# Kernel tuning notes

Measured on AMD Instinct MI355X. Metric: run time of the kernel, lower is better.

The kernel has to match this reference:

```python
import jax, jax.numpy as jnp
import numpy as np

N_EMBED = 1024
N_HEAD = 16
HEAD_DIM = N_EMBED // N_HEAD


def setup_inputs() -> dict:
    key = jax.random.key(0)
    k1, k2, k3, k4, k5 = jax.random.split(key, 5)
    x = jax.random.normal(k1, (4, 2048, N_EMBED), dtype=jnp.float32)
    s = 1.0 / np.sqrt(N_EMBED)
    W_attn = jax.random.normal(k2, (N_EMBED, 3 * N_EMBED), dtype=jnp.float32) * s
    b_attn = jnp.zeros((3 * N_EMBED,), dtype=jnp.float32)
    W_proj = jax.random.normal(k3, (N_EMBED, N_EMBED), dtype=jnp.float32) * s
    b_proj = jnp.zeros((N_EMBED,), dtype=jnp.float32)
    return {"x": x, "W_attn": W_attn, "b_attn": b_attn, "W_proj": W_proj, "b_proj": b_proj}


def reference(x, W_attn, b_attn, W_proj, b_proj):
    B, T, C = x.shape
    qkv = x @ W_attn + b_attn  # [B, T, 3C]
    q, k, v = jnp.split(qkv, 3, axis=2)
    # [B, H, T, D]
    q = q.reshape(B, T, N_HEAD, HEAD_DIM).transpose(0, 2, 1, 3)
    k = k.reshape(B, T, N_HEAD, HEAD_DIM).transpose(0, 2, 1, 3)
    v = v.reshape(B, T, N_HEAD, HEAD_DIM).transpose(0, 2, 1, 3)
    scale = 1.0 / np.sqrt(HEAD_DIM)
    scores = jnp.einsum('bhqd,bhkd->bhqk', q, k) * scale
    causal = jnp.tril(jnp.ones((T, T), dtype=bool))
    scores = jnp.where(causal[None, None], scores, -jnp.inf)
    attn = jax.nn.softmax(scores, axis=-1)
    y = jnp.einsum('bhqk,bhkd->bhqd', attn, v)
    y = y.transpose(0, 2, 1, 3).reshape(B, T, C)
    return y @ W_proj + b_proj
```

## Files before the change

### kernel.cpp

```cpp
#include <hip/hip_runtime.h>

typedef unsigned short u16;
typedef unsigned int u32;
typedef unsigned long long u64;
typedef __attribute__((ext_vector_type(8))) __bf16 b8;
typedef __attribute__((ext_vector_type(4))) float f32x4;

#define T_SEQ 2048
#define NB 4
#define NH 16
#define HD 64
#define CEMB 1024
#define M_ROWS (NB * T_SEQ)
#define Q_PRESCALE 0.18033688011112042f

__device__ __forceinline__ u16 f2bf(float f) {
  union { float f; unsigned int u; } v; v.f = f;
  unsigned int r = v.u + 0x7FFFu + ((v.u >> 16) & 1u);
  return (u16)(r >> 16);
}

__device__ __forceinline__ u32 pk2bf(float a, float b) {
  __bf16 x = (__bf16)a, y = (__bf16)b;
  return (u32)*(u16*)&x | ((u32)*(u16*)&y << 16);
}

__device__ __forceinline__ void gl_lds16(const u16* g, u16* l) {
  __builtin_amdgcn_global_load_lds(
      (const __attribute__((address_space(1))) unsigned int*)g,
      (__attribute__((address_space(3))) unsigned int*)l, 16, 0, 0);
}

#define BARRIER() __builtin_amdgcn_s_barrier()
#define LGKM0() do { asm volatile("s_waitcnt lgkmcnt(0)" ::: "memory"); \
                     __builtin_amdgcn_sched_barrier(0); } while (0)
#define VMCNT4() asm volatile("s_waitcnt vmcnt(4)" ::: "memory")
#define VMCNT2() asm volatile("s_waitcnt vmcnt(2)" ::: "memory")
#define VMCNT0() asm volatile("s_waitcnt vmcnt(0)" ::: "memory")

__global__ void k_convert(const float* __restrict__ in, u16* __restrict__ out, int n4) {
  int i = blockIdx.x * blockDim.x + threadIdx.x;
  int stride = gridDim.x * blockDim.x;
  for (; i < n4; i += stride) {
    float4 v = ((const float4*)in)[i];
    ushort4 o;
    o.x = f2bf(v.x); o.y = f2bf(v.y); o.z = f2bf(v.z); o.w = f2bf(v.w);
    ((ushort4*)out)[i] = o;
  }
}

__global__ __launch_bounds__(256) void k_transpose(const float* __restrict__ W,
                                                   u16* __restrict__ Wt, int K, int N) {
  __shared__ u16 t[64][65];
  int k0 = blockIdx.y * 64, n0 = blockIdx.x * 64;
  int tx = threadIdx.x & 63, ty = threadIdx.x >> 6;
  for (int i = ty; i < 64; i += 4)
    t[i][tx] = f2bf(W[(size_t)(k0 + i) * N + n0 + tx]);
  __syncthreads();
  for (int i = ty; i < 64; i += 4)
    Wt[(size_t)(n0 + i) * K + k0 + tx] = t[tx][i];
}

template <int MODE, int BNU>
__global__ __launch_bounds__(512, 2) void k_gemm8(const u16* __restrict__ A,
                                                  const u16* __restrict__ Bt,
                                                  const float* __restrict__ bias,
                                                  u16* __restrict__ out_bf,
                                                  float* __restrict__ out_f,
                                                  u16* __restrict__ vt,
                                                  int M, int N, int K, int mstripe) {
  __shared__ u16 sA[2][16384];
  __shared__ u16 sB[2][BNU * 4096];
  constexpr int NI = BNU / 2;
  const int tid = threadIdx.x;
  const int lane = tid & 63;
  const int wid = tid >> 6;
  const int wm = wid >> 2;
  const int wn = wid & 3;
  const int fr = lane & 15;
  const int g = lane >> 4;

  const int xcd = blockIdx.x & 7;
  const int idx = blockIdx.x >> 3;
  const int mt = xcd * mstripe + (idx % mstripe);
  const int nt = idx / mstripe;
  const int row0 = mt * 256, col0 = nt * (BNU * 64);
  const int NT = K >> 6;

  const int kswz = ((lane & 7) ^ ((lane >> 3) & 7)) * 8;
  const u16* gA = A + (size_t)(row0 + wid * 8 + (lane >> 3)) * K + kswz;
  const u16* gB = Bt + (size_t)(col0 + wid * 8 + (lane >> 3)) * K + kswz;

#define SGA(buf, T, u) gl_lds16(gA + (size_t)(u) * 64 * K + (size_t)(T) * 64, \
                                &sA[buf][(u) * 4096 + wid * 512])
#define SGB(buf, T, u) gl_lds16(gB + (size_t)(u) * 64 * K + (size_t)(T) * 64, \
                                &sB[buf][(u) * 4096 + wid * 512])
#define RDA(dst, rowe, ks)                                                     \
  { int row_ = (rowe);                                                         \
    dst = *(const b8*)&sA[bufc][row_ * 64 + ((((ks)*4 + g) ^ (row_ & 7)) << 3)]; }
#define RDB(dst, cole, ks)                                                     \
  { int col_ = (cole);                                                         \
    dst = *(const b8*)&sB[bufc][col_ * 64 + ((((ks)*4 + g) ^ (col_ & 7)) << 3)]; }

  f32x4 acc[8][BNU] = {};
  b8 aF[4][2], bF0[NI][2], bF1[NI][2];

#pragma unroll
  for (int u = 0; u < BNU; ++u) SGB(0, 0, u);
  SGA(0, 0, 0); SGA(0, 0, 2);
  SGA(0, 0, 1); SGA(0, 0, 3);
  SGA(1, 1, 0); SGA(1, 1, 2);
  VMCNT4();
  BARRIER();
  __builtin_amdgcn_sched_barrier(0);

#pragma unroll 2
  for (int T = 0; T < NT; ++T) {
    const int bufc = T & 1, bufn = bufc ^ 1;
    const bool st1 = (T + 1 < NT), st2 = (T + 2 < NT);

#pragma unroll
    for (int mi = 0; mi < 4; ++mi)
#pragma unroll
      for (int ks = 0; ks < 2; ++ks) RDA(aF[mi][ks], wm * 128 + mi * 16 + fr, ks);
#pragma unroll
    for (int ni = 0; ni < NI; ++ni)
#pragma unroll
      for (int ks = 0; ks < 2; ++ks) RDB(bF0[ni][ks], wn * (BNU * 16) + ni * 16 + fr, ks);
    if (st1) { SGB(bufn, T + 1, 0); SGB(bufn, T + 1, 1); }
    else VMCNT0();
    BARRIER(); LGKM0();
    __builtin_amdgcn_s_setprio(1);
#pragma unroll
    for (int mi = 0; mi < 4; ++mi)
#pragma unroll
      for (int ni = 0; ni < NI; ++ni)
#pragma unroll
        for (int ks = 0; ks < 2; ++ks)
          acc[mi][ni] = __builtin_amdgcn_mfma_f32_16x16x32_bf16(aF[mi][ks], bF0[ni][ks], acc[mi][ni], 0, 0, 0);
    __builtin_amdgcn_s_setprio(0);
    __builtin_amdgcn_sched_barrier(0);
    BARRIER();

#pragma unroll
    for (int ni = 0; ni < NI; ++ni)
#pragma unroll
      for (int ks = 0; ks < 2; ++ks) RDB(bF1[ni][ks], wn * (BNU * 16) + (NI + ni) * 16 + fr, ks);
    if (BNU == 4 && st1) { SGB(bufn, T + 1, 2); SGB(bufn, T + 1, 3); }
    if constexpr (BNU == 4) { VMCNT4(); } else { VMCNT2(); }
    BARRIER(); LGKM0();
    __builtin_amdgcn_s_setprio(1);
#pragma unroll
    for (int mi = 0; mi < 4; ++mi)
#pragma unroll
      for (int ni = 0; ni < NI; ++ni)
#pragma unroll
        for (int ks = 0; ks < 2; ++ks)
          acc[mi][NI + ni] = __builtin_amdgcn_mfma_f32_16x16x32_bf16(aF[mi][ks], bF1[ni][ks], acc[mi][NI + ni], 0, 0, 0);
    __builtin_amdgcn_s_setprio(0);
    __builtin_amdgcn_sched_barrier(0);
    BARRIER();

#pragma unroll
    for (int mi = 0; mi < 4; ++mi)
#pragma unroll
      for (int ks = 0; ks < 2; ++ks) RDA(aF[mi][ks], wm * 128 + 64 + mi * 16 + fr, ks);
    if (st2) { SGA(bufc, T + 2, 0); SGA(bufc, T + 2, 2); }
    BARRIER(); LGKM0();
    __builtin_amdgcn_s_setprio(1);
#pragma unroll
    for (int mi = 0; mi < 4; ++mi)
#pragma unroll
      for (int ni = 0; ni < NI; ++ni)
#pragma unroll
        for (int ks = 0; ks < 2; ++ks)
          acc[4 + mi][ni] = __builtin_amdgcn_mfma_f32_16x16x32_bf16(aF[mi][ks], bF0[ni][ks], acc[4 + mi][ni], 0, 0, 0);
    __builtin_amdgcn_s_setprio(0);
    __builtin_amdgcn_sched_barrier(0);
    BARRIER();

    if (st1) { SGA(bufn, T + 1, 1); SGA(bufn, T + 1, 3); }
    VMCNT4();
    BARRIER();
    __builtin_amdgcn_sched_barrier(0);
    __builtin_amdgcn_s_setprio(1);
#pragma unroll
    for (int mi = 0; mi < 4; ++mi)
#pragma unroll
      for (int ni = 0; ni < NI; ++ni)
#pragma unroll
        for (int ks = 0; ks < 2; ++ks)
          acc[4 + mi][NI + ni] = __builtin_amdgcn_mfma_f32_16x16x32_bf16(aF[mi][ks], bF1[ni][ks], acc[4 + mi][NI + ni], 0, 0, 0);
    __builtin_amdgcn_s_setprio(0);
    __builtin_amdgcn_sched_barrier(0);
    BARRIER();
  }
#undef SGA
#undef SGB
#undef RDA
#undef RDB

  const int fg = lane >> 4;
  if (MODE != 2) {
#pragma unroll
    for (int ni = 0; ni < BNU; ++ni) {
      int col = col0 + wn * (BNU * 16) + ni * 16 + fr;
      float bv = bias[col];
#pragma unroll
      for (int mi = 0; mi < 8; ++mi) {
#pragma unroll
        for (int r = 0; r < 4; ++r) {
          int row = row0 + wm * 128 + mi * 16 + fg * 4 + r;
          float v = acc[mi][ni][r] + bv;
          if (MODE == 0) {
            float sc = (col < CEMB) ? Q_PRESCALE : 1.0f;
            out_bf[(size_t)row * (2 * CEMB) + col] = f2bf(v * sc);
          } else {
            out_f[(size_t)row * N + col] = v;
          }
        }
      }
    }
  } else {
    u16* st = (u16*)sA;
    const int bq = row0 >> 11;
    const int t0g = row0 & (T_SEQ - 1);
#pragma unroll
    for (int pass = 0; pass < 2; ++pass) {
      __syncthreads();
      if ((wn >> 1) == pass) {
#pragma unroll
        for (int nn = 0; nn < BNU; ++nn) {
          const int hdl = (wn & 1) * 32 + nn * 16 + fr;
          const float bv = bias[col0 + pass * 64 + hdl];
#pragma unroll
          for (int mi = 0; mi < 8; ++mi) {
            const int tl = wm * 128 + mi * 16 + fg * 4;
#pragma unroll
            for (int rp = 0; rp < 2; ++rp) {
              u32 pk = pk2bf(acc[mi][nn][2 * rp] + bv, acc[mi][nn][2 * rp + 1] + bv);
              *(u32*)&st[hdl * 280 + tl + 2 * rp] = pk;
            }
          }
        }
      }
      __syncthreads();
      const int hd_r = tid >> 3;
      const int ck = tid & 7;
      u16* vrow = vt + ((size_t)(bq * (NH * HD) + col0 + pass * 64 + hd_r)) * T_SEQ + t0g;
#pragma unroll
      for (int j = 0; j < 4; ++j) {
        const int chunk = ck + 8 * j;
        f32x4 d = *(const f32x4*)&st[hd_r * 280 + chunk * 8];
        *(f32x4*)&vrow[chunk * 8] = d;
      }
    }
  }
}

__global__ __launch_bounds__(256) void k_attn(const u16* __restrict__ qk,
                                              const u16* __restrict__ vtg,
                                              u16* __restrict__ y) {
  __shared__ __align__(16) u16 kt_s[2][64 * 64];
  __shared__ __align__(16) u16 vt_s[2][64 * 64];
  __shared__ __align__(16) char pl_s[4][2048];

  const int lane = threadIdx.x & 63;
  const int wave = threadIdx.x >> 6;
  const int tid = threadIdx.x;
  const int g = lane >> 4, c = lane & 15;

  const int xcd = blockIdx.x & 7;
  const int idx = blockIdx.x >> 3;
  const int bh = xcd * 8 + (idx & 7);
  const int pr = idx >> 3;
  const int b = bh >> 4, h = bh & 15;

  char* plw = pl_s[wave];
  char* plA = plw + c * 128;
  const int b3 = c >> 3;
  const int e2 = (c & 7) << 1;
  const int sb = g + b3 * 8;

  b8 ones_frag;
#pragma unroll
  for (int e = 0; e < 8; ++e) ones_frag[e] = (c == 0) ? (__bf16)1.0f : (__bf16)0.0f;

  const int srow = tid >> 3;
  const int scc = (tid & 7) ^ (srow & 7);
  const u16* ksrc0 = qk + ((size_t)(b * T_SEQ) + srow) * (2 * CEMB) + CEMB + h * HD + scc * 8;
  const u16* vsrc0 = vtg + ((size_t)(bh * HD) + srow) * T_SEQ + scc * 8;

#define STAGE(t, bb)                                                    \
  {                                                                     \
    const u16* ks_ = ksrc0 + (size_t)(t) * 64 * (2 * CEMB);             \
    const u16* vs_ = vsrc0 + (t) * 64;                                  \
    gl_lds16(ks_, &kt_s[bb][wave * 512]);                               \
    gl_lds16(ks_ + 32 * (2 * CEMB), &kt_s[bb][wave * 512 + 2048]);      \
    gl_lds16(vs_, &vt_s[bb][wave * 512]);                               \
    gl_lds16(vs_ + 32 * T_SEQ, &vt_s[bb][wave * 512 + 2048]);           \
  }

#pragma unroll 1
  for (int seg = 0; seg < 2; ++seg) {
    const int tt = seg ? pr : (15 - pr);
    const int qA = tt * 128 + wave * 16;
    const int qB = qA + 64;

    const u16* qrowA = qk + (size_t)(b * T_SEQ + qA + c) * (2 * CEMB) + h * HD + g * 8;
    const b8 qfA0 = *(const b8*)qrowA;
    const b8 qfA1 = *(const b8*)(qrowA + 32);
    const u16* qrowB = qrowA + (size_t)64 * (2 * CEMB);
    const b8 qfB0 = *(const b8*)qrowB;
    const b8 qfB1 = *(const b8*)(qrowB + 32);

    float mA = -3e38f, mB = -3e38f;
    f32x4 oA[4] = {}, oB[4] = {};
    f32x4 o4A = {0.f, 0.f, 0.f, 0.f}, o4B = {0.f, 0.f, 0.f, 0.f};

    const int nt_tiles = 2 * tt + 2;
    int cur = 0;
    STAGE(0, 0);
    __syncthreads();

    for (int t = 0; t < nt_tiles; ++t) {
      if (t + 1 < nt_tiles) STAGE(t + 1, cur ^ 1);
      const int k0 = t * 64;
      const bool lastt = (t == nt_tiles - 1);
      const bool sndl = (t == nt_tiles - 2);
      const u16* kt = kt_s[cur];
      const u16* vtl = vt_s[cur];

      f32x4 sA[4] = {{0.f,0.f,0.f,0.f},{0.f,0.f,0.f,0.f},{0.f,0.f,0.f,0.f},{0.f,0.f,0.f,0.f}};
      f32x4 sB[4] = {{0.f,0.f,0.f,0.f},{0.f,0.f,0.f,0.f},{0.f,0.f,0.f,0.f},{0.f,0.f,0.f,0.f}};
      __builtin_amdgcn_s_setprio(1);
#pragma unroll
      for (int n = 0; n < 4; ++n) {
        const bool needA = (!lastt) && (!sndl || n <= wave);
        const bool needB = (!lastt) || (n <= wave);
        if (needA || needB) {
          const b8 kf0 = *(const b8*)&kt[(n * 16 + c) * 64 + ((g ^ (c & 7)) << 3)];
          const b8 kf1 = *(const b8*)&kt[(n * 16 + c) * 64 + (((4 + g) ^ (c & 7)) << 3)];
          if (needA) {
            sA[n] = __builtin_amdgcn_mfma_f32_16x16x32_bf16(kf0, qfA0, sA[n], 0, 0, 0);
            sA[n] = __builtin_amdgcn_mfma_f32_16x16x32_bf16(kf1, qfA1, sA[n], 0, 0, 0);
          }
          if (needB) {
            sB[n] = __builtin_amdgcn_mfma_f32_16x16x32_bf16(kf0, qfB0, sB[n], 0, 0, 0);
            sB[n] = __builtin_amdgcn_mfma_f32_16x16x32_bf16(kf1, qfB1, sB[n], 0, 0, 0);
          }
        }
      }
      __builtin_amdgcn_s_setprio(0);

      if (sndl) {
#pragma unroll
        for (int n = 0; n < 4; ++n)
#pragma unroll
          for (int r = 0; r < 4; ++r)
            if (k0 + n * 16 + g * 4 + r > qA + c) sA[n][r] = -3e38f;
      }
      if (lastt) {
#pragma unroll
        for (int n = 0; n < 4; ++n)
#pragma unroll
          for (int r = 0; r < 4; ++r)
            if (k0 + n * 16 + g * 4 + r > qB + c) sB[n][r] = -3e38f;
      }

      float rmA = -3e38f, rmB = -3e38f;
      if (!lastt) {
#pragma unroll
        for (int n = 0; n < 4; ++n)
#pragma unroll
          for (int r = 0; r < 4; ++r) rmA = fmaxf(rmA, sA[n][r]);
        rmA = fmaxf(rmA, __shfl_xor(rmA, 16));
        rmA = fmaxf(rmA, __shfl_xor(rmA, 32));
      }
#pragma unroll
      for (int n = 0; n < 4; ++n)
#pragma unroll
        for (int r = 0; r < 4; ++r) rmB = fmaxf(rmB, sB[n][r]);
      rmB = fmaxf(rmB, __shfl_xor(rmB, 16));
      rmB = fmaxf(rmB, __shfl_xor(rmB, 32));

      bool ok = (lastt || rmA <= mA + 8.0f) && (rmB <= mB + 8.0f);
      if (!__all(ok)) {
        float alA = 1.0f, alB;
        if (!lastt) {
          float mn = fmaxf(mA, rmA);
          alA = __builtin_amdgcn_exp2f(mA - mn);
          mA = mn;
        }
        {
          float mn = fmaxf(mB, rmB);
          alB = __builtin_amdgcn_exp2f(mB - mn);
          mB = mn;
        }
#pragma unroll
        for (int r = 0; r < 4; ++r) {
          int src = (lane & 48) + g * 4 + r;
          float aA = __shfl(alA, src);
          float aB = __shfl(alB, src);
#pragma unroll
          for (int nt = 0; nt < 4; ++nt) { oA[nt][r] *= aA; oB[nt][r] *= aB; }
          o4A[r] *= aA; o4B[r] *= aB;
        }
      }

      if (!lastt) {
#pragma unroll
        for (int n = 0; n < 4; ++n) {
          u32 lo = pk2bf(__builtin_amdgcn_exp2f(sA[n][0] - mA),
                         __builtin_amdgcn_exp2f(sA[n][1] - mA));
          u32 hi = pk2bf(__builtin_amdgcn_exp2f(sA[n][2] - mA),
                         __builtin_amdgcn_exp2f(sA[n][3] - mA));
          *(u64*)(plA + ((((4 * n + sb) & 15) ^ e2) << 3)) = ((u64)hi << 32) | lo;
        }
      }
      u64 pbB[4];
#pragma unroll
      for (int n = 0; n < 4; ++n) {
        u32 lo = pk2bf(__builtin_amdgcn_exp2f(sB[n][0] - mB),
                       __builtin_amdgcn_exp2f(sB[n][1] - mB));
        u32 hi = pk2bf(__builtin_amdgcn_exp2f(sB[n][2] - mB),
                       __builtin_amdgcn_exp2f(sB[n][3] - mB));
        pbB[n] = ((u64)hi << 32) | lo;
      }

      b8 vb[2][4];
#pragma unroll
      for (int ks = 0; ks < 2; ++ks)
#pragma unroll
        for (int nt = 0; nt < 4; ++nt)
          vb[ks][nt] = *(const b8*)&vtl[(nt * 16 + c) * 64 + (((ks * 4 + g) ^ (c & 7)) << 3)];

      asm volatile("s_waitcnt lgkmcnt(0)" ::: "memory");
      __builtin_amdgcn_sched_barrier(0);

      if (!lastt) {
        __builtin_amdgcn_s_setprio(1);
#pragma unroll
        for (int ks = 0; ks < 2; ++ks) {
          const b8 paA = *(const b8*)(plA + ((((ks * 8 + 2 * g + 8 * b3) & 15) ^ e2) << 3));
          o4A = __builtin_amdgcn_mfma_f32_16x16x32_bf16(paA, ones_frag, o4A, 0, 0, 0);
#pragma unroll
          for (int nt = 0; nt < 4; ++nt)
            oA[nt] = __builtin_amdgcn_mfma_f32_16x16x32_bf16(paA, vb[ks][nt], oA[nt], 0, 0, 0);
        }
        __builtin_amdgcn_s_setprio(0);
      }

#pragma unroll
      for (int n = 0; n < 4; ++n)
        *(u64*)(plA + ((((4 * n + sb) & 15) ^ e2) << 3)) = pbB[n];
      asm volatile("s_waitcnt lgkmcnt(0)" ::: "memory");
      __builtin_amdgcn_sched_barrier(0);

      __builtin_amdgcn_s_setprio(1);
#pragma unroll
      for (int ks = 0; ks < 2; ++ks) {
        const b8 paB = *(const b8*)(plA + ((((ks * 8 + 2 * g + 8 * b3) & 15) ^ e2) << 3));
        o4B = __builtin_amdgcn_mfma_f32_16x16x32_bf16(paB, ones_frag, o4B, 0, 0, 0);
#pragma unroll
        for (int nt = 0; nt < 4; ++nt)
          oB[nt] = __builtin_amdgcn_mfma_f32_16x16x32_bf16(paB, vb[ks][nt], oB[nt], 0, 0, 0);
      }
      __builtin_amdgcn_s_setprio(0);

      __syncthreads();
      cur ^= 1;
    }

#pragma unroll
    for (int r = 0; r < 4; ++r) {
      float lA = __shfl(o4A[r], lane & 48);
      float lB = __shfl(o4B[r], lane & 48);
      float invA = 1.0f / lA;
      float invB = 1.0f / lB;
#pragma unroll
      for (int nt = 0; nt < 4; ++nt) {
        __bf16 va = (__bf16)(oA[nt][r] * invA);
        __bf16 vbv = (__bf16)(oB[nt][r] * invB);
        y[(size_t)(b * T_SEQ + qA + g * 4 + r) * CEMB + h * HD + nt * 16 + c] = *(u16*)&va;
        y[(size_t)(b * T_SEQ + qB + g * 4 + r) * CEMB + h * HD + nt * 16 + c] = *(u16*)&vbv;
      }
    }
  }
#undef STAGE
}

extern "C" void kernel_launch(void* const* d_in, const int* in_sizes, int n_in,
                              void* d_out, int out_size, void* d_ws, size_t ws_size,
                              hipStream_t stream) {
  const float* x = (const float*)d_in[0];
  const float* W_attn = (const float*)d_in[1];
  const float* b_attn = (const float*)d_in[2];
  const float* W_proj = (const float*)d_in[3];
  const float* b_proj = (const float*)d_in[4];
  float* out = (float*)d_out;

  char* ws = (char*)d_ws;
  u16* x_bf    = (u16*)(ws);
  u16* wattn_t = (u16*)(ws + 16777216);
  u16* wproj_t = (u16*)(ws + 23068672);
  u16* qk_bf   = (u16*)(ws + 25165824);
  u16* vt      = (u16*)(ws + 58720256);
  u16* y_bf    = (u16*)(ws + 75497472);

  k_convert<<<2048, 256, 0, stream>>>(x, x_bf, (NB * T_SEQ * CEMB) / 4);
  k_transpose<<<dim3(3 * CEMB / 64, CEMB / 64), 256, 0, stream>>>(W_attn, wattn_t, CEMB, 3 * CEMB);
  k_transpose<<<dim3(CEMB / 64, CEMB / 64), 256, 0, stream>>>(W_proj, wproj_t, CEMB, CEMB);
  k_gemm8<0, 4><<<256, 512, 0, stream>>>(x_bf, wattn_t, b_attn, qk_bf, nullptr, nullptr,
                                         M_ROWS, 2 * CEMB, CEMB, 4);
  k_gemm8<2, 2><<<256, 512, 0, stream>>>(x_bf, wattn_t + 2048 * CEMB, b_attn + 2 * CEMB,
                                         nullptr, nullptr, vt, M_ROWS, CEMB, CEMB, 4);
  k_attn<<<512, 256, 0, stream>>>(qk_bf, vt, y_bf);
  k_gemm8<1, 2><<<256, 512, 0, stream>>>(y_bf, wproj_t, b_proj, nullptr, out, nullptr,
                                         M_ROWS, CEMB, CEMB, 4);
}
```

Before: 194.1 us.

## Split attention blocks to one 64-row query tile per wave group

```diff
diff --git a/kernel.cpp b/kernel.cpp
--- a/kernel.cpp
+++ b/kernel.cpp
@@ -258,9 +258,9 @@
   }
 }
 
-__global__ __launch_bounds__(256) void k_attn(const u16* __restrict__ qk,
-                                              const u16* __restrict__ vtg,
-                                              u16* __restrict__ y) {
+__global__ __launch_bounds__(256, 4) void k_attn(const u16* __restrict__ qk,
+                                                 const u16* __restrict__ vtg,
+                                                 u16* __restrict__ y) {
   __shared__ __align__(16) u16 kt_s[2][64 * 64];
   __shared__ __align__(16) u16 vt_s[2][64 * 64];
   __shared__ __align__(16) char pl_s[4][2048];
@@ -303,129 +303,79 @@
 
 #pragma unroll 1
   for (int seg = 0; seg < 2; ++seg) {
-    const int tt = seg ? pr : (15 - pr);
-    const int qA = tt * 128 + wave * 16;
-    const int qB = qA + 64;
-
-    const u16* qrowA = qk + (size_t)(b * T_SEQ + qA + c) * (2 * CEMB) + h * HD + g * 8;
-    const b8 qfA0 = *(const b8*)qrowA;
-    const b8 qfA1 = *(const b8*)(qrowA + 32);
-    const u16* qrowB = qrowA + (size_t)64 * (2 * CEMB);
-    const b8 qfB0 = *(const b8*)qrowB;
-    const b8 qfB1 = *(const b8*)(qrowB + 32);
-
-    float mA = -3e38f, mB = -3e38f;
-    f32x4 oA[4] = {}, oB[4] = {};
-    f32x4 o4A = {0.f, 0.f, 0.f, 0.f}, o4B = {0.f, 0.f, 0.f, 0.f};
-
-    const int nt_tiles = 2 * tt + 2;
+    const int tt = seg ? pr : (31 - pr);
+    const int qW = tt * 64 + wave * 16;
+
+    const u16* qrow = qk + (size_t)(b * T_SEQ + qW + c) * (2 * CEMB) + h * HD + g * 8;
+    const b8 qf0 = *(const b8*)qrow;
+    const b8 qf1 = *(const b8*)(qrow + 32);
+
+    float m = -3e38f;
+    f32x4 o[4] = {};
+    f32x4 o4 = {0.f, 0.f, 0.f, 0.f};
+
+    const int ntt = tt + 1;
     int cur = 0;
     STAGE(0, 0);
     __syncthreads();
 
-    for (int t = 0; t < nt_tiles; ++t) {
-      if (t + 1 < nt_tiles) STAGE(t + 1, cur ^ 1);
+    for (int t = 0; t < ntt; ++t) {
+      if (t + 1 < ntt) STAGE(t + 1, cur ^ 1);
       const int k0 = t * 64;
-      const bool lastt = (t == nt_tiles - 1);
-      const bool sndl = (t == nt_tiles - 2);
+      const bool diag = (t == ntt - 1);
       const u16* kt = kt_s[cur];
       const u16* vtl = vt_s[cur];
 
-      f32x4 sA[4] = {{0.f,0.f,0.f,0.f},{0.f,0.f,0.f,0.f},{0.f,0.f,0.f,0.f},{0.f,0.f,0.f,0.f}};
-      f32x4 sB[4] = {{0.f,0.f,0.f,0.f},{0.f,0.f,0.f,0.f},{0.f,0.f,0.f,0.f},{0.f,0.f,0.f,0.f}};
+      f32x4 s[4] = {{0.f,0.f,0.f,0.f},{0.f,0.f,0.f,0.f},{0.f,0.f,0.f,0.f},{0.f,0.f,0.f,0.f}};
       __builtin_amdgcn_s_setprio(1);
 #pragma unroll
       for (int n = 0; n < 4; ++n) {
-        const bool needA = (!lastt) && (!sndl || n <= wave);
-        const bool needB = (!lastt) || (n <= wave);
-        if (needA || needB) {
+        if (!diag || n <= wave) {
           const b8 kf0 = *(const b8*)&kt[(n * 16 + c) * 64 + ((g ^ (c & 7)) << 3)];
           const b8 kf1 = *(const b8*)&kt[(n * 16 + c) * 64 + (((4 + g) ^ (c & 7)) << 3)];
-          if (needA) {
-            sA[n] = __builtin_amdgcn_mfma_f32_16x16x32_bf16(kf0, qfA0, sA[n], 0, 0, 0);
-            sA[n] = __builtin_amdgcn_mfma_f32_16x16x32_bf16(kf1, qfA1, sA[n], 0, 0, 0);
-          }
-          if (needB) {
-            sB[n] = __builtin_amdgcn_mfma_f32_16x16x32_bf16(kf0, qfB0, sB[n], 0, 0, 0);
-            sB[n] = __builtin_amdgcn_mfma_f32_16x16x32_bf16(kf1, qfB1, sB[n], 0, 0, 0);
-          }
+          s[n] = __builtin_amdgcn_mfma_f32_16x16x32_bf16(kf0, qf0, s[n], 0, 0, 0);
+          s[n] = __builtin_amdgcn_mfma_f32_16x16x32_bf16(kf1, qf1, s[n], 0, 0, 0);
         }
       }
       __builtin_amdgcn_s_setprio(0);
 
-      if (sndl) {
+      if (diag) {
 #pragma unroll
         for (int n = 0; n < 4; ++n)
 #pragma unroll
           for (int r = 0; r < 4; ++r)
-            if (k0 + n * 16 + g * 4 + r > qA + c) sA[n][r] = -3e38f;
-      }
-      if (lastt) {
-#pragma unroll
-        for (int n = 0; n < 4; ++n)
-#pragma unroll
-          for (int r = 0; r < 4; ++r)
-            if (k0 + n * 16 + g * 4 + r > qB + c) sB[n][r] = -3e38f;
-      }
-
-      float rmA = -3e38f, rmB = -3e38f;
-      if (!lastt) {
-#pragma unroll
-        for (int n = 0; n < 4; ++n)
-#pragma unroll
-          for (int r = 0; r < 4; ++r) rmA = fmaxf(rmA, sA[n][r]);
-        rmA = fmaxf(rmA, __shfl_xor(rmA, 16));
-        rmA = fmaxf(rmA, __shfl_xor(rmA, 32));
-      }
-#pragma unroll
-      for (int n = 0; n < 4; ++n)
-#pragma unroll
-        for (int r = 0; r < 4; ++r) rmB = fmaxf(rmB, sB[n][r]);
-      rmB = fmaxf(rmB, __shfl_xor(rmB, 16));
-      rmB = fmaxf(rmB, __shfl_xor(rmB, 32));
-
-      bool ok = (lastt || rmA <= mA + 8.0f) && (rmB <= mB + 8.0f);
-      if (!__all(ok)) {
-        float alA = 1.0f, alB;
-        if (!lastt) {
-          float mn = fmaxf(mA, rmA);
-          alA = __builtin_amdgcn_exp2f(mA - mn);
-          mA = mn;
-        }
-        {
-          float mn = fmaxf(mB, rmB);
-          alB = __builtin_amdgcn_exp2f(mB - mn);
-          mB = mn;
-        }
+            if (k0 + n * 16 + g * 4 + r > qW + c) s[n][r] = -3e38f;
+      }
+
+      float rm = fmaxf(fmaxf(fmaxf(s[0][0], s[0][1]), s[0][2]),
+                       fmaxf(fmaxf(s[0][3], s[1][0]), s[1][1]));
+      rm = fmaxf(rm, fmaxf(fmaxf(s[1][2], s[1][3]), s[2][0]));
+      rm = fmaxf(rm, fmaxf(fmaxf(s[2][1], s[2][2]), s[2][3]));
+      rm = fmaxf(rm, fmaxf(fmaxf(s[3][0], s[3][1]), fmaxf(s[3][2], s[3][3])));
+      rm = fmaxf(rm, __shfl_xor(rm, 16));
+      rm = fmaxf(rm, __shfl_xor(rm, 32));
+
+      if (!__all(rm <= m + 8.0f)) {
+        float mn = fmaxf(m, rm);
+        float al = __builtin_amdgcn_exp2f(m - mn);
+        m = mn;
 #pragma unroll
         for (int r = 0; r < 4; ++r) {
           int src = (lane & 48) + g * 4 + r;
-          float aA = __shfl(alA, src);
-          float aB = __shfl(alB, src);
-#pragma unroll
-          for (int nt = 0; nt < 4; ++nt) { oA[nt][r] *= aA; oB[nt][r] *= aB; }
-          o4A[r] *= aA; o4B[r] *= aB;
+          float a = __shfl(al, src);
+#pragma unroll
+          for (int nt = 0; nt < 4; ++nt) o[nt][r] *= a;
+          o4[r] *= a;
         }
       }
 
-      if (!lastt) {
-#pragma unroll
-        for (int n = 0; n < 4; ++n) {
-          u32 lo = pk2bf(__builtin_amdgcn_exp2f(sA[n][0] - mA),
-                         __builtin_amdgcn_exp2f(sA[n][1] - mA));
-          u32 hi = pk2bf(__builtin_amdgcn_exp2f(sA[n][2] - mA),
-                         __builtin_amdgcn_exp2f(sA[n][3] - mA));
-          *(u64*)(plA + ((((4 * n + sb) & 15) ^ e2) << 3)) = ((u64)hi << 32) | lo;
-        }
-      }
-      u64 pbB[4];
 #pragma unroll
       for (int n = 0; n < 4; ++n) {
-        u32 lo = pk2bf(__builtin_amdgcn_exp2f(sB[n][0] - mB),
-                       __builtin_amdgcn_exp2f(sB[n][1] - mB));
-        u32 hi = pk2bf(__builtin_amdgcn_exp2f(sB[n][2] - mB),
-                       __builtin_amdgcn_exp2f(sB[n][3] - mB));
-        pbB[n] = ((u64)hi << 32) | lo;
+        u32 lo = pk2bf(__builtin_amdgcn_exp2f(s[n][0] - m),
+                       __builtin_amdgcn_exp2f(s[n][1] - m));
+        u32 hi = pk2bf(__builtin_amdgcn_exp2f(s[n][2] - m),
+                       __builtin_amdgcn_exp2f(s[n][3] - m));
+        *(u64*)(plA + ((((4 * n + sb) & 15) ^ e2) << 3)) = ((u64)hi << 32) | lo;
       }
 
       b8 vb[2][4];
@@ -438,33 +388,14 @@
       asm volatile("s_waitcnt lgkmcnt(0)" ::: "memory");
       __builtin_amdgcn_sched_barrier(0);
 
-      if (!lastt) {
-        __builtin_amdgcn_s_setprio(1);
-#pragma unroll
-        for (int ks = 0; ks < 2; ++ks) {
-          const b8 paA = *(const b8*)(plA + ((((ks * 8 + 2 * g + 8 * b3) & 15) ^ e2) << 3));
-          o4A = __builtin_amdgcn_mfma_f32_16x16x32_bf16(paA, ones_frag, o4A, 0, 0, 0);
-#pragma unroll
-          for (int nt = 0; nt < 4; ++nt)
-            oA[nt] = __builtin_amdgcn_mfma_f32_16x16x32_bf16(paA, vb[ks][nt], oA[nt], 0, 0, 0);
-        }
-        __builtin_amdgcn_s_setprio(0);
-      }
-
-#pragma unroll
-      for (int n = 0; n < 4; ++n)
-        *(u64*)(plA + ((((4 * n + sb) & 15) ^ e2) << 3)) = pbB[n];
-      asm volatile("s_waitcnt lgkmcnt(0)" ::: "memory");
-      __builtin_amdgcn_sched_barrier(0);
-
       __builtin_amdgcn_s_setprio(1);
 #pragma unroll
       for (int ks = 0; ks < 2; ++ks) {
-        const b8 paB = *(const b8*)(plA + ((((ks * 8 + 2 * g + 8 * b3) & 15) ^ e2) << 3));
-        o4B = __builtin_amdgcn_mfma_f32_16x16x32_bf16(paB, ones_frag, o4B, 0, 0, 0);
+        const b8 pa = *(const b8*)(plA + ((((ks * 8 + 2 * g + 8 * b3) & 15) ^ e2) << 3));
+        o4 = __builtin_amdgcn_mfma_f32_16x16x32_bf16(pa, ones_frag, o4, 0, 0, 0);
 #pragma unroll
         for (int nt = 0; nt < 4; ++nt)
-          oB[nt] = __builtin_amdgcn_mfma_f32_16x16x32_bf16(paB, vb[ks][nt], oB[nt], 0, 0, 0);
+          o[nt] = __builtin_amdgcn_mfma_f32_16x16x32_bf16(pa, vb[ks][nt], o[nt], 0, 0, 0);
       }
       __builtin_amdgcn_s_setprio(0);
 
@@ -474,16 +405,12 @@
 
 #pragma unroll
     for (int r = 0; r < 4; ++r) {
-      float lA = __shfl(o4A[r], lane & 48);
-      float lB = __shfl(o4B[r], lane & 48);
-      float invA = 1.0f / lA;
-      float invB = 1.0f / lB;
+      float lr = __shfl(o4[r], lane & 48);
+      float inv = 1.0f / lr;
 #pragma unroll
       for (int nt = 0; nt < 4; ++nt) {
-        __bf16 va = (__bf16)(oA[nt][r] * invA);
-        __bf16 vbv = (__bf16)(oB[nt][r] * invB);
-        y[(size_t)(b * T_SEQ + qA + g * 4 + r) * CEMB + h * HD + nt * 16 + c] = *(u16*)&va;
-        y[(size_t)(b * T_SEQ + qB + g * 4 + r) * CEMB + h * HD + nt * 16 + c] = *(u16*)&vbv;
+        __bf16 ov = (__bf16)(o[nt][r] * inv);
+        y[(size_t)(b * T_SEQ + qW + g * 4 + r) * CEMB + h * HD + nt * 16 + c] = *(u16*)&ov;
       }
     }
   }
@@ -515,7 +442,7 @@
                                          M_ROWS, 2 * CEMB, CEMB, 4);
   k_gemm8<2, 2><<<256, 512, 0, stream>>>(x_bf, wattn_t + 2048 * CEMB, b_attn + 2 * CEMB,
                                          nullptr, nullptr, vt, M_ROWS, CEMB, CEMB, 4);
-  k_attn<<<512, 256, 0, stream>>>(qk_bf, vt, y_bf);
+  k_attn<<<1024, 256, 0, stream>>>(qk_bf, vt, y_bf);
   k_gemm8<1, 2><<<256, 512, 0, stream>>>(y_bf, wproj_t, b_proj, nullptr, out, nullptr,
                                          M_ROWS, CEMB, CEMB, 4);
 }
```

Result: faster. 184.4 us (-5.0%).
